# Performance work log

Hardware: AMD Instinct MI355X
Metric: run time of the kernel (lower is better)

## Reference

```python
import jax, jax.numpy as jnp
import numpy as np

B, IN_DIM, K, D = 8192, 1024, 2048, 256
TAU = 1.0
BN_EPS = 1e-5


def setup_inputs() -> dict:
    key = jax.random.key(0)
    ks = jax.random.split(key, 4)
    x = jax.random.normal(ks[0], (B, IN_DIM), dtype=jnp.float32)
    u = jax.random.uniform(ks[1], (B, K), dtype=jnp.float32)  # uniform for gumbel noise
    W = jax.random.normal(ks[2], (IN_DIM, D), dtype=jnp.float32) * 0.02
    b = jnp.zeros((D,), dtype=jnp.float32)
    gamma = jnp.ones((D,), dtype=jnp.float32)
    beta = jnp.zeros((D,), dtype=jnp.float32)
    E = jax.random.normal(ks[3], (K, D), dtype=jnp.float32)  # nn.Embedding default N(0,1)
    return {"x": x, "u": u, "W": W, "b": b, "gamma": gamma, "beta": beta, "E": E}


def reference(x, u, W, b, gamma, beta, E):
    # classifier + BatchNorm1d (training mode: batch stats, biased variance)
    h = x @ W + b                                   # [B, D]
    mu = jnp.mean(h, axis=0)
    var = jnp.var(h, axis=0)
    h = (h - mu) * jax.lax.rsqrt(var + BN_EPS) * gamma + beta
    # negative squared euclidean distance via ||h||^2 - 2 h.E^T + ||e||^2 (GEMM form,
    # avoids materializing [B, K, D])
    h2 = jnp.sum(h * h, axis=-1, keepdims=True)     # [B, 1]
    e2 = jnp.sum(E * E, axis=-1)                    # [K]
    logits = -(h2 - 2.0 * (h @ E.T) + e2)           # [B, K]
    # gumbel-softmax (soft) with tau
    g = -jnp.log(-jnp.log(u + 1e-10) + 1e-10)
    assignments = jax.nn.softmax((logits + g) / TAU, axis=-1)  # [B, K]
    z = assignments @ E                             # [B, D]
    probs = jax.nn.softmax(logits, axis=-1)
    return probs, z
```

## Files before the change

kernel.cpp:

```cpp
#include <hip/hip_runtime.h>
#include <math.h>

#define B_SZ 8192
#define IN_DIM 1024
#define K_CB 2048
#define D_SZ 256
#define BN_EPS 1e-5f

typedef _Float16 f16;
typedef _Float16 f16x8 __attribute__((ext_vector_type(8)));
typedef _Float16 f16x4 __attribute__((ext_vector_type(4)));
typedef float    f32x4 __attribute__((ext_vector_type(4)));

#define GLOAD_LDS16(g, l) __builtin_amdgcn_global_load_lds(                      \
    (const __attribute__((address_space(1))) unsigned int*)(g),                  \
    (__attribute__((address_space(3))) unsigned int*)(l), 16, 0, 0)

template<int BM, int BN, int BK, int EPI, bool A32>
__global__ __launch_bounds__(256) void gemm_mfma(
    const void* __restrict__ Aptr, int lda,
    const f16* __restrict__ Bptr, int ldb,
    void* __restrict__ Cptr, int ldc, int Kdim,
    const float* __restrict__ bias)
{
    constexpr int G    = BK / 8;
    constexpr int MASK = G - 1;
    constexpr int WM = BM / 2, WN = BN / 2;
    constexpr int FM = WM / 16, FN = WN / 16;
    constexpr int CH_A = BM * G;
    constexpr int CH_B = BN * G;

    __shared__ char lds[(BM + BN) * BK * 2];
    char* As = lds;
    char* Bs = lds + BM * BK * 2;

    const int tid  = threadIdx.x;
    const int w    = tid >> 6, lane = tid & 63;
    const int wm   = w >> 1,   wn   = w & 1;
    const int row0 = blockIdx.x * BM;
    const int col0 = blockIdx.y * BN;

    f32x4 acc[FM][FN] = {};

    for (int k0 = 0; k0 < Kdim; k0 += BK) {
        #pragma unroll
        for (int i = 0; i < CH_B / 256; ++i) {
            const int base = (i * 4 + w) * 64;
            const int s = base + lane;
            const int r = s / G, c = s % G;
            const f16* src = Bptr + (size_t)(col0 + r) * ldb + k0 + ((c ^ (r & MASK)) * 8);
            GLOAD_LDS16(src, Bs + base * 16);
        }
        if (!A32) {
            #pragma unroll
            for (int i = 0; i < CH_A / 256; ++i) {
                const int base = (i * 4 + w) * 64;
                const int s = base + lane;
                const int r = s / G, c = s % G;
                const f16* src = (const f16*)Aptr + (size_t)(row0 + r) * lda + k0 + ((c ^ (r & MASK)) * 8);
                GLOAD_LDS16(src, As + base * 16);
            }
        } else {
            #pragma unroll
            for (int i = 0; i < CH_A / 256; ++i) {
                const int s = i * 256 + tid;
                const int r = s / G, c = s % G;
                const float* src = (const float*)Aptr + (size_t)(row0 + r) * lda + k0 + c * 8;
                const float4 v0 = ((const float4*)src)[0];
                const float4 v1 = ((const float4*)src)[1];
                f16x8 d;
                d[0] = (f16)v0.x; d[1] = (f16)v0.y; d[2] = (f16)v0.z; d[3] = (f16)v0.w;
                d[4] = (f16)v1.x; d[5] = (f16)v1.y; d[6] = (f16)v1.z; d[7] = (f16)v1.w;
                *(f16x8*)(As + (r * G + (c ^ (r & MASK))) * 16) = d;
            }
        }
        __syncthreads();

        #pragma unroll
        for (int kk = 0; kk < BK / 32; ++kk) {
            f16x8 af[FM], bf[FN];
            #pragma unroll
            for (int m = 0; m < FM; ++m) {
                const int r = wm * WM + m * 16 + (lane & 15);
                const int g = (kk * 4 + (lane >> 4)) ^ (r & MASK);
                af[m] = *(const f16x8*)(As + r * (BK * 2) + g * 16);
            }
            #pragma unroll
            for (int n = 0; n < FN; ++n) {
                const int r = wn * WN + n * 16 + (lane & 15);
                const int g = (kk * 4 + (lane >> 4)) ^ (r & MASK);
                bf[n] = *(const f16x8*)(Bs + r * (BK * 2) + g * 16);
            }
            #pragma unroll
            for (int m = 0; m < FM; ++m)
                #pragma unroll
                for (int n = 0; n < FN; ++n)
                    acc[m][n] = __builtin_amdgcn_mfma_f32_16x16x32_f16(af[m], bf[n], acc[m][n], 0, 0, 0);
        }
        __syncthreads();
    }

    #pragma unroll
    for (int m = 0; m < FM; ++m) {
        const int rbase = row0 + wm * WM + m * 16 + (lane >> 4) * 4;
        #pragma unroll
        for (int n = 0; n < FN; ++n) {
            const int c = col0 + wn * WN + n * 16 + (lane & 15);
            #pragma unroll
            for (int j = 0; j < 4; ++j) {
                const float v = acc[m][n][j];
                if (EPI == 0) {
                    ((float*)Cptr)[(size_t)(rbase + j) * ldc + c] = v;
                } else {
                    ((f16*)Cptr)[(size_t)(rbase + j) * ldc + c] = (f16)(v + bias[c]);
                }
            }
        }
    }
}

#define LVP 2052

__global__ __launch_bounds__(512, 2) void fused_sm(
    const f16* __restrict__ h16, const f16* __restrict__ E16,
    const float* __restrict__ e2v, const float* __restrict__ u,
    const float* __restrict__ scale, const float* __restrict__ shift,
    float* __restrict__ probs, f16* __restrict__ assign16)
{
    __shared__ __align__(16) char lds_raw[16 * LVP * 4];
    f16* Bs0 = (f16*)lds_raw;
    f16* Bs1 = Bs0 + 128 * 256;
    float* lv_lds = (float*)lds_raw;

    const int tid  = threadIdx.x;
    const int w    = tid >> 6, lane = tid & 63;
    const int q    = lane >> 4, r16 = lane & 15;
    const int row0 = blockIdx.x * 16;
    const int colL = w * 16 + r16;
    const int trow = tid >> 5;
    const int cg   = tid & 31;

    const float* urow = u + (size_t)(row0 + trow) * K_CB + cg * 4;
    float4 uu[16];
    #pragma unroll
    for (int n = 0; n < 16; ++n) uu[n] = *(const float4*)(urow + n * 128);

    f16x8 af[8];
    {
        const f16* hrow = h16 + (size_t)(row0 + r16) * D_SZ + q * 8;
        #pragma unroll
        for (int kk = 0; kk < 8; ++kk) {
            const f16x8 raw = *(const f16x8*)(hrow + kk * 32);
            const float4 scA = *(const float4*)(scale + kk * 32 + q * 8);
            const float4 scB = *(const float4*)(scale + kk * 32 + q * 8 + 4);
            const float4 shA = *(const float4*)(shift + kk * 32 + q * 8);
            const float4 shB = *(const float4*)(shift + kk * 32 + q * 8 + 4);
            f16x8 d;
            d[0] = (f16)fmaf((float)raw[0], scA.x, shA.x);
            d[1] = (f16)fmaf((float)raw[1], scA.y, shA.y);
            d[2] = (f16)fmaf((float)raw[2], scA.z, shA.z);
            d[3] = (f16)fmaf((float)raw[3], scA.w, shA.w);
            d[4] = (f16)fmaf((float)raw[4], scB.x, shB.x);
            d[5] = (f16)fmaf((float)raw[5], scB.y, shB.y);
            d[6] = (f16)fmaf((float)raw[6], scB.z, shB.z);
            d[7] = (f16)fmaf((float)raw[7], scB.w, shB.w);
            af[kk] = d;
        }
    }

    f32x4 acc[16];
    #pragma unroll
    for (int n = 0; n < 16; ++n) acc[n] = (f32x4){0.f, 0.f, 0.f, 0.f};
    f16x4 gv[16];

    #pragma unroll
    for (int i = 0; i < 8; ++i) {
        const int base = (i * 8 + w) * 64;
        const int s = base + lane;
        const int r = s >> 5, cgg = s & 31;
        GLOAD_LDS16(E16 + (size_t)r * D_SZ + ((cgg ^ (r & 31)) * 8), Bs0 + base * 8);
    }

    #pragma unroll
    for (int c = 0; c < 16; ++c) {
        f16* buf = (c & 1) ? Bs1 : Bs0;
        f16* nbuf = (c & 1) ? Bs0 : Bs1;
        if (c < 15) {
            #pragma unroll
            for (int i = 0; i < 8; ++i) {
                const int base = (i * 8 + w) * 64;
                const int s = base + lane;
                const int r = s >> 5, cgg = s & 31;
                GLOAD_LDS16(E16 + (size_t)((c + 1) * 128 + r) * D_SZ + ((cgg ^ (r & 31)) * 8),
                            nbuf + base * 8);
            }
            asm volatile("s_waitcnt vmcnt(8)" ::: "memory");
        } else {
            asm volatile("s_waitcnt vmcnt(0)" ::: "memory");
        }
        __builtin_amdgcn_s_barrier();
        __builtin_amdgcn_sched_barrier(0);
        #pragma unroll
        for (int kk = 0; kk < 8; ++kk) {
            const int gb = (kk * 4 + q) ^ (colL & 31);
            const f16x8 bf = *(const f16x8*)(buf + colL * 256 + gb * 8);
            acc[c] = __builtin_amdgcn_mfma_f32_16x16x32_f16(af[kk], bf, acc[c], 0, 0, 0);
        }
        __builtin_amdgcn_sched_barrier(0);
        __builtin_amdgcn_s_barrier();
        __builtin_amdgcn_sched_barrier(0);
        if (c >= 1 && c <= 4) {
            const int b0 = (c - 1) * 4;
            #pragma unroll
            for (int nn = 0; nn < 4; ++nn) {
                const float4 u4 = uu[b0 + nn];
                const float ua[4] = {u4.x, u4.y, u4.z, u4.w};
                #pragma unroll
                for (int e = 0; e < 4; ++e)
                    gv[b0 + nn][e] = (f16)(-__logf(-__logf(ua[e] + 1e-10f) + 1e-10f));
            }
        }
    }
    __syncthreads();

    #pragma unroll
    for (int n = 0; n < 16; ++n) {
        const float ec = e2v[n * 128 + colL];
        #pragma unroll
        for (int j = 0; j < 4; ++j) {
            lv_lds[(q * 4 + j) * LVP + n * 128 + colL] = 2.f * acc[n][j] - ec;
        }
    }
    __syncthreads();

    const float* lrow = lv_lds + trow * LVP + cg * 4;

    float m1 = -1e30f, m2 = -1e30f;
    #pragma unroll
    for (int n = 0; n < 16; ++n) {
        const f32x4 l4 = *(const f32x4*)(lrow + n * 128);
        #pragma unroll
        for (int e = 0; e < 4; ++e) {
            m1 = fmaxf(m1, l4[e]);
            m2 = fmaxf(m2, l4[e] + (float)gv[n][e]);
        }
    }
    #pragma unroll
    for (int off = 1; off < 32; off <<= 1) {
        m1 = fmaxf(m1, __shfl_xor(m1, off));
        m2 = fmaxf(m2, __shfl_xor(m2, off));
    }

    float s1 = 0.f, s2 = 0.f;
    f32x4 p1[16];
    #pragma unroll
    for (int n = 0; n < 16; ++n) {
        const f32x4 l4 = *(const f32x4*)(lrow + n * 128);
        #pragma unroll
        for (int e = 0; e < 4; ++e) {
            const float a = __expf(l4[e] - m1);
            const float b = a * __expf((float)gv[n][e] + m1 - m2);
            p1[n][e] = a; gv[n][e] = (f16)b;
            s1 += a; s2 += b;
        }
    }
    #pragma unroll
    for (int off = 1; off < 32; off <<= 1) {
        s1 += __shfl_xor(s1, off);
        s2 += __shfl_xor(s2, off);
    }
    const float r1 = 1.f / s1;
    const float r2 = 1.f / s2;

    float* prow = probs + (size_t)(row0 + trow) * K_CB + cg * 4;
    f16* arow = assign16 + (size_t)(row0 + trow) * K_CB + cg * 4;
    #pragma unroll
    for (int n = 0; n < 16; ++n) {
        float4 o;
        o.x = p1[n][0] * r1; o.y = p1[n][1] * r1;
        o.z = p1[n][2] * r1; o.w = p1[n][3] * r1;
        *(float4*)(prow + n * 128) = o;
        f16x4 a4;
        #pragma unroll
        for (int e = 0; e < 4; ++e) a4[e] = (f16)((float)gv[n][e] * r2);
        *(f16x4*)(arow + n * 128) = a4;
    }
}

__global__ __launch_bounds__(256) void conv_WT(const float* __restrict__ W, f16* __restrict__ WT)
{
    const int r = blockIdx.x, c = threadIdx.x;
    WT[c * 1024 + r] = (f16)W[r * 256 + c];
}

__global__ __launch_bounds__(256) void conv_E2(const float* __restrict__ E,
                                               f16* __restrict__ E16, f16* __restrict__ ET,
                                               float* __restrict__ e2)
{
    const int r = blockIdx.x, c = threadIdx.x;
    const int wave = c >> 6, lane = c & 63;
    const float v = E[r * 256 + c];
    E16[r * 256 + c] = (f16)v;
    ET[c * 2048 + r] = (f16)v;
    float ss = v * v;
    #pragma unroll
    for (int off = 32; off > 0; off >>= 1) ss += __shfl_down(ss, off);
    __shared__ float s4[4];
    if (lane == 0) s4[wave] = ss;
    __syncthreads();
    if (c == 0) e2[r] = s4[0] + s4[1] + s4[2] + s4[3];
}

__global__ __launch_bounds__(256) void bn_partial(const f16* __restrict__ h16, float* __restrict__ part)
{
    const int d = threadIdx.x;
    const int blk = blockIdx.x;
    const int r0 = blk * (B_SZ / 128);
    float s = 0.f, sq = 0.f;
    for (int r = r0; r < r0 + (B_SZ / 128); ++r) {
        const float v = (float)h16[(size_t)r * D_SZ + d];
        s += v; sq += v * v;
    }
    part[blk * 512 + d]       = s;
    part[blk * 512 + 256 + d] = sq;
}

__global__ __launch_bounds__(256) void bn_finalize(
    const float* __restrict__ part, const float* __restrict__ gamma, const float* __restrict__ beta,
    float* __restrict__ scale, float* __restrict__ shift)
{
    const int d = threadIdx.x;
    float s = 0.f, sq = 0.f;
    for (int b = 0; b < 128; ++b) { s += part[b * 512 + d]; sq += part[b * 512 + 256 + d]; }
    const float mu  = s / (float)B_SZ;
    const float var = sq / (float)B_SZ - mu * mu;
    const float sc  = gamma[d] * rsqrtf(var + BN_EPS);
    scale[d] = sc;
    shift[d] = beta[d] - mu * sc;
}

extern "C" void kernel_launch(void* const* d_in, const int* in_sizes, int n_in,
                              void* d_out, int out_size, void* d_ws, size_t ws_size,
                              hipStream_t stream)
{
    const float* x     = (const float*)d_in[0];
    const float* u     = (const float*)d_in[1];
    const float* W     = (const float*)d_in[2];
    const float* bias  = (const float*)d_in[3];
    const float* gamma = (const float*)d_in[4];
    const float* beta  = (const float*)d_in[5];
    const float* E     = (const float*)d_in[6];

    float* probs = (float*)d_out;
    float* z     = probs + (size_t)B_SZ * K_CB;

    char* ws = (char*)d_ws;
    f16* assign16 = (f16*)ws;  ws += (size_t)B_SZ * K_CB * 2;
    f16* h16 = (f16*)ws;       ws += (size_t)B_SZ * D_SZ * 2;
    f16* WT16 = (f16*)ws;      ws += (size_t)D_SZ * IN_DIM * 2;
    f16* E16 = (f16*)ws;       ws += (size_t)K_CB * D_SZ * 2;
    f16* ET16 = (f16*)ws;      ws += (size_t)D_SZ * K_CB * 2;
    float* part = (float*)ws;  ws += 128 * 512 * 4;
    float* scale = (float*)ws; ws += D_SZ * 4;
    float* shift = (float*)ws; ws += D_SZ * 4;
    float* e2 = (float*)ws;    ws += K_CB * 4;

    conv_WT<<<IN_DIM, 256, 0, stream>>>(W, WT16);
    conv_E2<<<K_CB, 256, 0, stream>>>(E, E16, ET16, e2);

    {
        dim3 g(B_SZ / 64, D_SZ / 64);
        gemm_mfma<64, 64, 64, 1, true><<<g, 256, 0, stream>>>(
            x, IN_DIM, WT16, IN_DIM, h16, D_SZ, IN_DIM, bias);
    }
    bn_partial<<<128, 256, 0, stream>>>(h16, part);
    bn_finalize<<<1, 256, 0, stream>>>(part, gamma, beta, scale, shift);

    fused_sm<<<B_SZ / 16, 512, 0, stream>>>(h16, E16, e2, u, scale, shift, probs, assign16);

    {
        dim3 g(B_SZ / 64, D_SZ / 64);
        gemm_mfma<64, 64, 128, 0, false><<<g, 256, 0, stream>>>(
            assign16, K_CB, ET16, K_CB, z, D_SZ, K_CB, nullptr);
    }
}
```

Baseline: 126.2 us.

## Halve rows per softmax block, single-buffer E tiles, compute gumbel noise in softmax phase

The fused distance/softmax kernel now handles 8 rows per block instead of 16. That shrinks the LDS footprint to about half, so more blocks can be resident per CU. The E tile is single-buffered with a full wait each chunk, and the gumbel noise is computed during the softmax pass, one wave per row, instead of being prefetched and overlapped with the MFMA loop. The trade-off is heavy: the 16-row MFMA still computes 16 rows with half discarded, total E traffic doubles, and the load/compute overlap is lost. The last block also reads h16 rows past the batch end.

Measured after the change: 165.3 us. 1.31x slower.

```diff
diff --git a/kernel.cpp b/kernel.cpp
--- a/kernel.cpp
+++ b/kernel.cpp
@@ -127,23 +127,15 @@
     const float* __restrict__ scale, const float* __restrict__ shift,
     float* __restrict__ probs, f16* __restrict__ assign16)
 {
-    __shared__ __align__(16) char lds_raw[16 * LVP * 4];
-    f16* Bs0 = (f16*)lds_raw;
-    f16* Bs1 = Bs0 + 128 * 256;
+    __shared__ __align__(16) char lds_raw[8 * LVP * 4];
+    f16* Bs = (f16*)lds_raw;
     float* lv_lds = (float*)lds_raw;
 
     const int tid  = threadIdx.x;
     const int w    = tid >> 6, lane = tid & 63;
     const int q    = lane >> 4, r16 = lane & 15;
-    const int row0 = blockIdx.x * 16;
+    const int row0 = blockIdx.x * 8;
     const int colL = w * 16 + r16;
-    const int trow = tid >> 5;
-    const int cg   = tid & 31;
-
-    const float* urow = u + (size_t)(row0 + trow) * K_CB + cg * 4;
-    float4 uu[16];
-    #pragma unroll
-    for (int n = 0; n < 16; ++n) uu[n] = *(const float4*)(urow + n * 128);
 
     f16x8 af[8];
     {
@@ -171,91 +163,74 @@
     f32x4 acc[16];
     #pragma unroll
     for (int n = 0; n < 16; ++n) acc[n] = (f32x4){0.f, 0.f, 0.f, 0.f};
-    f16x4 gv[16];
-
-    #pragma unroll
-    for (int i = 0; i < 8; ++i) {
-        const int base = (i * 8 + w) * 64;
-        const int s = base + lane;
-        const int r = s >> 5, cgg = s & 31;
-        GLOAD_LDS16(E16 + (size_t)r * D_SZ + ((cgg ^ (r & 31)) * 8), Bs0 + base * 8);
-    }
 
     #pragma unroll
     for (int c = 0; c < 16; ++c) {
-        f16* buf = (c & 1) ? Bs1 : Bs0;
-        f16* nbuf = (c & 1) ? Bs0 : Bs1;
-        if (c < 15) {
-            #pragma unroll
-            for (int i = 0; i < 8; ++i) {
-                const int base = (i * 8 + w) * 64;
-                const int s = base + lane;
-                const int r = s >> 5, cgg = s & 31;
-                GLOAD_LDS16(E16 + (size_t)((c + 1) * 128 + r) * D_SZ + ((cgg ^ (r & 31)) * 8),
-                            nbuf + base * 8);
-            }
-            asm volatile("s_waitcnt vmcnt(8)" ::: "memory");
-        } else {
-            asm volatile("s_waitcnt vmcnt(0)" ::: "memory");
-        }
+        if (c > 0) __builtin_amdgcn_s_barrier();
+        #pragma unroll
+        for (int i = 0; i < 8; ++i) {
+            const int base = (i * 8 + w) * 64;
+            const int s = base + lane;
+            const int r = s >> 5, cgg = s & 31;
+            GLOAD_LDS16(E16 + (size_t)(c * 128 + r) * D_SZ + ((cgg ^ (r & 31)) * 8),
+                        Bs + base * 8);
+        }
+        asm volatile("s_waitcnt vmcnt(0)" ::: "memory");
         __builtin_amdgcn_s_barrier();
         __builtin_amdgcn_sched_barrier(0);
         #pragma unroll
         for (int kk = 0; kk < 8; ++kk) {
             const int gb = (kk * 4 + q) ^ (colL & 31);
-            const f16x8 bf = *(const f16x8*)(buf + colL * 256 + gb * 8);
+            const f16x8 bf = *(const f16x8*)(Bs + colL * 256 + gb * 8);
             acc[c] = __builtin_amdgcn_mfma_f32_16x16x32_f16(af[kk], bf, acc[c], 0, 0, 0);
         }
         __builtin_amdgcn_sched_barrier(0);
-        __builtin_amdgcn_s_barrier();
-        __builtin_amdgcn_sched_barrier(0);
-        if (c >= 1 && c <= 4) {
-            const int b0 = (c - 1) * 4;
-            #pragma unroll
-            for (int nn = 0; nn < 4; ++nn) {
-                const float4 u4 = uu[b0 + nn];
-                const float ua[4] = {u4.x, u4.y, u4.z, u4.w};
-                #pragma unroll
-                for (int e = 0; e < 4; ++e)
-                    gv[b0 + nn][e] = (f16)(-__logf(-__logf(ua[e] + 1e-10f) + 1e-10f));
-            }
-        }
     }
     __syncthreads();
 
-    #pragma unroll
-    for (int n = 0; n < 16; ++n) {
-        const float ec = e2v[n * 128 + colL];
-        #pragma unroll
-        for (int j = 0; j < 4; ++j) {
-            lv_lds[(q * 4 + j) * LVP + n * 128 + colL] = 2.f * acc[n][j] - ec;
+    if (q < 2) {
+        #pragma unroll
+        for (int n = 0; n < 16; ++n) {
+            const float ec = e2v[n * 128 + colL];
+            #pragma unroll
+            for (int j = 0; j < 4; ++j) {
+                lv_lds[(q * 4 + j) * LVP + n * 128 + colL] = 2.f * acc[n][j] - ec;
+            }
         }
     }
     __syncthreads();
 
+    const int trow = w;
+    const int cg   = lane;
     const float* lrow = lv_lds + trow * LVP + cg * 4;
+    const float* urow = u + (size_t)(row0 + trow) * K_CB + cg * 4;
 
     float m1 = -1e30f, m2 = -1e30f;
-    #pragma unroll
-    for (int n = 0; n < 16; ++n) {
-        const f32x4 l4 = *(const f32x4*)(lrow + n * 128);
+    f16x4 gv[8];
+    #pragma unroll
+    for (int n = 0; n < 8; ++n) {
+        const float4 u4 = *(const float4*)(urow + n * 256);
+        const f32x4 l4 = *(const f32x4*)(lrow + n * 256);
+        const float ua[4] = {u4.x, u4.y, u4.z, u4.w};
         #pragma unroll
         for (int e = 0; e < 4; ++e) {
+            const float g = -__logf(-__logf(ua[e] + 1e-10f) + 1e-10f);
+            gv[n][e] = (f16)g;
             m1 = fmaxf(m1, l4[e]);
             m2 = fmaxf(m2, l4[e] + (float)gv[n][e]);
         }
     }
     #pragma unroll
-    for (int off = 1; off < 32; off <<= 1) {
+    for (int off = 1; off < 64; off <<= 1) {
         m1 = fmaxf(m1, __shfl_xor(m1, off));
         m2 = fmaxf(m2, __shfl_xor(m2, off));
     }
 
     float s1 = 0.f, s2 = 0.f;
-    f32x4 p1[16];
-    #pragma unroll
-    for (int n = 0; n < 16; ++n) {
-        const f32x4 l4 = *(const f32x4*)(lrow + n * 128);
+    f32x4 p1[8];
+    #pragma unroll
+    for (int n = 0; n < 8; ++n) {
+        const f32x4 l4 = *(const f32x4*)(lrow + n * 256);
         #pragma unroll
         for (int e = 0; e < 4; ++e) {
             const float a = __expf(l4[e] - m1);
@@ -265,7 +240,7 @@
         }
     }
     #pragma unroll
-    for (int off = 1; off < 32; off <<= 1) {
+    for (int off = 1; off < 64; off <<= 1) {
         s1 += __shfl_xor(s1, off);
         s2 += __shfl_xor(s2, off);
     }
@@ -275,15 +250,15 @@
     float* prow = probs + (size_t)(row0 + trow) * K_CB + cg * 4;
     f16* arow = assign16 + (size_t)(row0 + trow) * K_CB + cg * 4;
     #pragma unroll
-    for (int n = 0; n < 16; ++n) {
+    for (int n = 0; n < 8; ++n) {
         float4 o;
         o.x = p1[n][0] * r1; o.y = p1[n][1] * r1;
         o.z = p1[n][2] * r1; o.w = p1[n][3] * r1;
-        *(float4*)(prow + n * 128) = o;
+        *(float4*)(prow + n * 256) = o;
         f16x4 a4;
         #pragma unroll
         for (int e = 0; e < 4; ++e) a4[e] = (f16)((float)gv[n][e] * r2);
-        *(f16x4*)(arow + n * 128) = a4;
+        *(f16x4*)(arow + n * 256) = a4;
     }
 }
 
@@ -376,7 +351,7 @@
     bn_partial<<<128, 256, 0, stream>>>(h16, part);
     bn_finalize<<<1, 256, 0, stream>>>(part, gamma, beta, scale, shift);
 
-    fused_sm<<<B_SZ / 16, 512, 0, stream>>>(h16, E16, e2, u, scale, shift, probs, assign16);
+    fused_sm<<<B_SZ / 8, 512, 0, stream>>>(h16, E16, e2, u, scale, shift, probs, assign16);
 
     {
         dim3 g(B_SZ / 64, D_SZ / 64);
```
